# Performance work log

Hardware: AMD Instinct MI355X
Metric: run time of the kernel (lower is better)

The kernel has to match this reference:

```python
import jax, jax.numpy as jnp
import numpy as np

B, N, F, H, E = 8, 10000, 256, 128, 320000
P_DROP = 0.5

def setup_inputs() -> dict:
    key = jax.random.key(0)
    kx, ku, kr, kc, kv, kw = jax.random.split(key, 6)
    x = jax.random.normal(kx, (B, N, F), dtype=jnp.float32)
    drop_u = jax.random.uniform(ku, (B, N, F), dtype=jnp.float32)
    rows = jax.random.randint(kr, (B, E), 0, N, dtype=jnp.int64)
    cols = jax.random.randint(kc, (B, E), 0, N, dtype=jnp.int64)
    vals = jax.random.uniform(kv, (B, E), dtype=jnp.float32)
    weight = jax.random.normal(kw, (F, H), dtype=jnp.float32)
    return {"x": x, "drop_u": drop_u, "rows": rows, "cols": cols, "vals": vals, "weight": weight}

def _spmm(rows, cols, vals, dense):
    # out[r] += vals * dense[c]  -> A @ dense for one graph
    gathered = vals[:, None] * dense[cols]          # [E, H]
    return jax.ops.segment_sum(gathered, rows, num_segments=N)  # [N, H]

def reference(x, drop_u, rows, cols, vals, weight):
    # inverted dropout, p=0.5
    mask = (drop_u > P_DROP).astype(x.dtype)
    xd = x * mask * (1.0 / (1.0 - P_DROP))          # [B, N, F]
    xw = jnp.einsum('bnf,fh->bnh', xd, weight)      # [B, N, H]
    out = jax.vmap(_spmm)(rows, cols, vals, xw)     # [B, N, H]
    return out
```

## Files before the change

kernel.cpp:

```cpp
#include <hip/hip_runtime.h>
#include <hip/hip_bf16.h>

#define DEVINL __device__ __forceinline__

constexpr int Bb = 8;
constexpr int Nn = 10000;
constexpr int Ff = 256;
constexpr int Hh = 128;
constexpr int Ee = 320000;
constexpr int Mm = Bb * Nn;

constexpr int CHUNK = 64;
constexpr int NCH = (Nn + CHUNK - 1) / CHUNK;
constexpr int CAP = 2560;
constexpr int GPB = 40;
constexpr int EPG = Ee / GPB;
constexpr int TW_BLOCKS = (Ff * Hh) / 256;

typedef __attribute__((ext_vector_type(8))) short short8;
typedef __attribute__((ext_vector_type(4))) float float4v;
typedef __attribute__((ext_vector_type(4))) unsigned short ushort4v;

DEVINL float b2f(unsigned short s) {
    unsigned int u = ((unsigned int)s) << 16;
    float f;
    __builtin_memcpy(&f, &u, 4);
    return f;
}
DEVINL unsigned short f2b(float f) {
    unsigned int u;
    __builtin_memcpy(&u, &f, 4);
    unsigned int r = (u + 0x7fffu + ((u >> 16) & 1u)) >> 16;
    return (unsigned short)r;
}
DEVINL float i2f(int i) {
    float f;
    __builtin_memcpy(&f, &i, 4);
    return f;
}

__global__ __launch_bounds__(256) void bucket_kernel(const int* __restrict__ rows,
                                                     const int* __restrict__ cols,
                                                     const float* __restrict__ vals,
                                                     int* __restrict__ cur,
                                                     int2* __restrict__ bkt,
                                                     const float* __restrict__ w,
                                                     unsigned short* __restrict__ wT) {
    int t = threadIdx.x;
    if (blockIdx.x >= Bb * GPB) {
        int idx = (blockIdx.x - Bb * GPB) * 256 + t;
        if (idx < Ff * Hh) {
            int h = idx / Ff, k = idx % Ff;
            wT[idx] = f2b(w[(size_t)k * Hh + h]);
        }
        return;
    }
    __shared__ int lcnt[NCH];
    __shared__ int lbase[NCH];
    int raw = blockIdx.x;
    int b = raw & 7;
    int g = raw >> 3;
    const int base = b * Ee + g * EPG;

    for (int j = t; j < NCH; j += 256) lcnt[j] = 0;
    __syncthreads();
    for (int i = t; i < EPG; i += 256)
        atomicAdd(&lcnt[rows[base + i] >> 6], 1);
    __syncthreads();
    for (int j = t; j < NCH; j += 256)
        lbase[j] = atomicAdd(&cur[b * NCH + j], lcnt[j]);
    __syncthreads();
    for (int j = t; j < NCH; j += 256) lcnt[j] = 0;
    __syncthreads();
    for (int i = t; i < EPG; i += 256) {
        int r = rows[base + i];
        int bk = r >> 6;
        int off = atomicAdd(&lcnt[bk], 1);
        int pos = lbase[bk] + off;
        if (pos < CAP) {
            int c = cols[base + i];
            float vf = vals[base + i];
            int vb;
            __builtin_memcpy(&vb, &vf, 4);
            bkt[(size_t)(b * NCH + bk) * CAP + pos] = make_int2(c | ((r & 63) << 20), vb);
        }
    }
}

__global__ __launch_bounds__(256, 3) void gemm_kernel(const float* __restrict__ x,
                                                      const float* __restrict__ u,
                                                      const unsigned short* __restrict__ wT,
                                                      unsigned short* __restrict__ xw) {
    __shared__ unsigned short sA[64 * 136];
    __shared__ unsigned short sB[128 * 136];
    int t = threadIdx.x;
    int wave = t >> 6, lane = t & 63;
    int n = lane & 15, q = lane >> 4;
    int m0 = blockIdx.x * 64;

    float4v acc[8];
#pragma unroll
    for (int i = 0; i < 8; i++) acc[i] = {0.f, 0.f, 0.f, 0.f};

    for (int kh = 0; kh < 2; kh++) {
#pragma unroll
        for (int i = 0; i < 8; i++) {
            int idx = t + i * 256;
            int row = idx >> 5;
            int c4 = idx & 31;
            const float* xp = x + (size_t)(m0 + row) * Ff + kh * 128 + c4 * 4;
            const float* up = u + (size_t)(m0 + row) * Ff + kh * 128 + c4 * 4;
            float4 xv = *(const float4*)xp;
            float4 uv = *(const float4*)up;
            ushort4v a;
            a.x = f2b(uv.x > 0.5f ? xv.x * 2.0f : 0.0f);
            a.y = f2b(uv.y > 0.5f ? xv.y * 2.0f : 0.0f);
            a.z = f2b(uv.z > 0.5f ? xv.z * 2.0f : 0.0f);
            a.w = f2b(uv.w > 0.5f ? xv.w * 2.0f : 0.0f);
            *(ushort4v*)(&sA[row * 136 + c4 * 4]) = a;
        }
#pragma unroll
        for (int i = 0; i < 8; i++) {
            int idx = t + i * 256;
            int h = idx >> 4;
            int kc = idx & 15;
            short8 bv = *(const short8*)(wT + (size_t)h * Ff + kh * 128 + kc * 8);
            *(short8*)(&sB[h * 136 + kc * 8]) = bv;
        }
        __syncthreads();
#pragma unroll
        for (int k0 = 0; k0 < 128; k0 += 32) {
            short8 af = *(const short8*)(&sA[(wave * 16 + n) * 136 + k0 + q * 8]);
#pragma unroll
            for (int tt = 0; tt < 8; tt++) {
                short8 bf = *(const short8*)(&sB[(tt * 16 + n) * 136 + k0 + q * 8]);
                acc[tt] = __builtin_amdgcn_mfma_f32_16x16x32_bf16(af, bf, acc[tt], 0, 0, 0);
            }
        }
        __syncthreads();
    }
#pragma unroll
    for (int tt = 0; tt < 8; tt++) {
#pragma unroll
        for (int r = 0; r < 4; r++) {
            int row = m0 + wave * 16 + q * 4 + r;
            int col = tt * 16 + n;
            xw[(size_t)row * Hh + col] = f2b(acc[tt][r]);
        }
    }
}

__global__ __launch_bounds__(256) void spmm_kernel(const int* __restrict__ cur,
                                                   const int2* __restrict__ bkt,
                                                   const unsigned short* __restrict__ xw,
                                                   float* __restrict__ out) {
    __shared__ int2 sedge[CAP];
    __shared__ int scnt[CHUNK];
    __shared__ int soff[CHUNK];
    __shared__ int scur[CHUNK];
    int raw = blockIdx.x;
    int blk = (raw & 7) * NCH + (raw >> 3);
    int b = blk / NCH, ch = blk % NCH;
    int t = threadIdx.x, w = t >> 6, lane = t & 63;

    if (t < CHUNK) scnt[t] = 0;
    __syncthreads();
    int cnt = cur[blk];
    if (cnt > CAP) cnt = CAP;
    const int2* pe = bkt + (size_t)blk * CAP;

    for (int i = t; i < cnt; i += 256)
        atomicAdd(&scnt[pe[i].x >> 20], 1);
    __syncthreads();
    if (w == 0) {
        int v = scnt[lane];
        int s = v;
#pragma unroll
        for (int d = 1; d < 64; d <<= 1) {
            int o = __shfl_up(s, d);
            if (lane >= d) s += o;
        }
        soff[lane] = s - v;
        scur[lane] = s - v;
    }
    __syncthreads();
    for (int i = t; i < cnt; i += 256) {
        int2 e = pe[i];
        int pos = atomicAdd(&scur[e.x >> 20], 1);
        sedge[pos] = e;
    }
    __syncthreads();

    const unsigned short* xwb = xw + (size_t)b * Nn * Hh;
    for (int rr = 0; rr < 16; rr++) {
        int rl = w * 16 + rr;
        int r = ch * CHUNK + rl;
        if (r >= Nn) break;
        int off = soff[rl];
        int rcnt = scnt[rl];

        float a0[8], a1[8];
#pragma unroll
        for (int k = 0; k < 8; k++) { a0[k] = 0.f; a1[k] = 0.f; }

        for (int c0 = 0; c0 < rcnt; c0 += 64) {
            int rem = rcnt - c0;
            if (rem > 64) rem = 64;
            int2 e = make_int2(0, 0);
            if (lane < rem) e = sedge[off + c0 + lane];
            int rrp = (rem + 7) & ~7;
            for (int j = 0; j < rrp; j += 8) {
#pragma unroll
                for (int k = 0; k < 8; k++) {
                    int c = __builtin_amdgcn_readlane(e.x, j + k) & 0xFFFFF;
                    float v = i2f(__builtin_amdgcn_readlane(e.y, j + k));
                    unsigned int two = *(const unsigned int*)(xwb + (size_t)c * Hh + lane * 2);
                    a0[k] += v * b2f((unsigned short)(two & 0xffffu));
                    a1[k] += v * b2f((unsigned short)(two >> 16));
                }
            }
        }
        float s0 = ((a0[0] + a0[1]) + (a0[2] + a0[3])) + ((a0[4] + a0[5]) + (a0[6] + a0[7]));
        float s1 = ((a1[0] + a1[1]) + (a1[2] + a1[3])) + ((a1[4] + a1[5]) + (a1[6] + a1[7]));
        float2 res;
        res.x = s0;
        res.y = s1;
        *(float2*)(out + ((size_t)b * Nn + r) * Hh + lane * 2) = res;
    }
}

extern "C" void kernel_launch(void* const* d_in, const int* in_sizes, int n_in,
                              void* d_out, int out_size, void* d_ws, size_t ws_size,
                              hipStream_t stream) {
    const float* x    = (const float*)d_in[0];
    const float* du   = (const float*)d_in[1];
    const int*   rows = (const int*)d_in[2];
    const int*   cols = (const int*)d_in[3];
    const float* vals = (const float*)d_in[4];
    const float* w    = (const float*)d_in[5];
    float*       out  = (float*)d_out;

    char* p = (char*)d_ws;
    unsigned short* xw = (unsigned short*)p; p += (size_t)Mm * Hh * 2;
    unsigned short* wT = (unsigned short*)p; p += (size_t)Ff * Hh * 2;
    int* cur   = (int*)p; p += (size_t)Bb * NCH * 4;
    int2* bkt  = (int2*)p; p += (size_t)Bb * NCH * CAP * 8;

    hipMemsetAsync(cur, 0, (size_t)Bb * NCH * 4, stream);
    bucket_kernel<<<Bb * GPB + TW_BLOCKS, 256, 0, stream>>>(rows, cols, vals, cur, bkt, w, wT);
    gemm_kernel<<<Mm / 64, 256, 0, stream>>>(x, du, wT, xw);
    spmm_kernel<<<Bb * NCH, 256, 0, stream>>>(cur, bkt, xw, out);
}
```

Baseline: 336.0 us.

## Replace chunked bucket sort with exact per-row CSR build and one-wave-per-row SpMM

Replaces the 64-row chunk bucketing, which had a fixed capacity and an in-block re-sort, with a global per-row histogram, a per-graph prefix scan and an atomic scatter into an exact CSR array. The SpMM then assigns one wave per row, stages up to 160 edges in shared memory and falls back to global reads for longer rows. Column indices are pre-shifted into byte offsets to save address arithmetic. This removes the capacity truncation and the per-block sorting work, at the cost of two extra kernel launches, global atomics on individual rows and many small blocks.

```diff
diff --git a/kernel.cpp b/kernel.cpp
--- a/kernel.cpp
+++ b/kernel.cpp
@@ -10,12 +10,10 @@
 constexpr int Ee = 320000;
 constexpr int Mm = Bb * Nn;
 
-constexpr int CHUNK = 64;
-constexpr int NCH = (Nn + CHUNK - 1) / CHUNK;
-constexpr int CAP = 2560;
 constexpr int GPB = 40;
 constexpr int EPG = Ee / GPB;
 constexpr int TW_BLOCKS = (Ff * Hh) / 256;
+constexpr int SCAP = 160;
 
 typedef __attribute__((ext_vector_type(8))) short short8;
 typedef __attribute__((ext_vector_type(4))) float float4v;
@@ -38,14 +36,23 @@
     __builtin_memcpy(&f, &i, 4);
     return f;
 }
-
-__global__ __launch_bounds__(256) void bucket_kernel(const int* __restrict__ rows,
-                                                     const int* __restrict__ cols,
-                                                     const float* __restrict__ vals,
-                                                     int* __restrict__ cur,
-                                                     int2* __restrict__ bkt,
-                                                     const float* __restrict__ w,
-                                                     unsigned short* __restrict__ wT) {
+DEVINL float lo_bf(unsigned int two) {
+    unsigned int u = two << 16;
+    float f;
+    __builtin_memcpy(&f, &u, 4);
+    return f;
+}
+DEVINL float hi_bf(unsigned int two) {
+    unsigned int u = two & 0xffff0000u;
+    float f;
+    __builtin_memcpy(&f, &u, 4);
+    return f;
+}
+
+__global__ __launch_bounds__(256) void hist_kernel(const int* __restrict__ rows,
+                                                   int* __restrict__ cnt,
+                                                   const float* __restrict__ w,
+                                                   unsigned short* __restrict__ wT) {
     int t = threadIdx.x;
     if (blockIdx.x >= Bb * GPB) {
         int idx = (blockIdx.x - Bb * GPB) * 256 + t;
@@ -55,35 +62,83 @@
         }
         return;
     }
-    __shared__ int lcnt[NCH];
-    __shared__ int lbase[NCH];
     int raw = blockIdx.x;
     int b = raw & 7;
     int g = raw >> 3;
     const int base = b * Ee + g * EPG;
-
-    for (int j = t; j < NCH; j += 256) lcnt[j] = 0;
+    int* cb = cnt + b * Nn;
+    for (int i = t; i < EPG; i += 256)
+        atomicAdd(&cb[rows[base + i]], 1);
+}
+
+__global__ __launch_bounds__(1024) void scan_kernel(const int* __restrict__ cnt,
+                                                    int* __restrict__ off,
+                                                    int* __restrict__ cur) {
+    __shared__ int wsum[16];
+    int b = blockIdx.x;
+    int t = threadIdx.x;
+    int lane = t & 63, w = t >> 6;
+    const int base = b * Nn;
+    int local[10];
+    int s = 0;
+    int r0 = t * 10;
+#pragma unroll
+    for (int j = 0; j < 10; j++) {
+        int r = r0 + j;
+        int c = (r < Nn) ? cnt[base + r] : 0;
+        local[j] = s;
+        s += c;
+    }
+    int incl = s;
+#pragma unroll
+    for (int d = 1; d < 64; d <<= 1) {
+        int o = __shfl_up(incl, d);
+        if (lane >= d) incl += o;
+    }
+    if (lane == 63) wsum[w] = incl;
     __syncthreads();
-    for (int i = t; i < EPG; i += 256)
-        atomicAdd(&lcnt[rows[base + i] >> 6], 1);
+    if (w == 0) {
+        int v = (lane < 16) ? wsum[lane] : 0;
+        int sc = v;
+#pragma unroll
+        for (int d = 1; d < 16; d <<= 1) {
+            int o = __shfl_up(sc, d);
+            if (lane >= d) sc += o;
+        }
+        if (lane < 16) wsum[lane] = sc - v;
+    }
     __syncthreads();
-    for (int j = t; j < NCH; j += 256)
-        lbase[j] = atomicAdd(&cur[b * NCH + j], lcnt[j]);
-    __syncthreads();
-    for (int j = t; j < NCH; j += 256) lcnt[j] = 0;
-    __syncthreads();
+    int tbase = b * Ee + wsum[w] + (incl - s);
+#pragma unroll
+    for (int j = 0; j < 10; j++) {
+        int r = r0 + j;
+        if (r < Nn) {
+            int o = tbase + local[j];
+            off[base + r] = o;
+            cur[base + r] = o;
+        }
+    }
+}
+
+__global__ __launch_bounds__(256) void scatter_kernel(const int* __restrict__ rows,
+                                                      const int* __restrict__ cols,
+                                                      const float* __restrict__ vals,
+                                                      int* __restrict__ cur,
+                                                      int2* __restrict__ csr) {
+    int raw = blockIdx.x;
+    int b = raw & 7;
+    int g = raw >> 3;
+    int t = threadIdx.x;
+    const int base = b * Ee + g * EPG;
+    int* cb = cur + b * Nn;
     for (int i = t; i < EPG; i += 256) {
         int r = rows[base + i];
-        int bk = r >> 6;
-        int off = atomicAdd(&lcnt[bk], 1);
-        int pos = lbase[bk] + off;
-        if (pos < CAP) {
-            int c = cols[base + i];
-            float vf = vals[base + i];
-            int vb;
-            __builtin_memcpy(&vb, &vf, 4);
-            bkt[(size_t)(b * NCH + bk) * CAP + pos] = make_int2(c | ((r & 63) << 20), vb);
-        }
+        int c = cols[base + i];
+        float vf = vals[base + i];
+        int vb;
+        __builtin_memcpy(&vb, &vf, 4);
+        int pos = atomicAdd(&cb[r], 1);
+        csr[pos] = make_int2(c << 8, vb);
     }
 }
 
@@ -150,83 +205,56 @@
     }
 }
 
-__global__ __launch_bounds__(256) void spmm_kernel(const int* __restrict__ cur,
-                                                   const int2* __restrict__ bkt,
+__global__ __launch_bounds__(256) void spmm_kernel(const int* __restrict__ off,
+                                                   const int* __restrict__ cnt,
+                                                   const int2* __restrict__ csr,
                                                    const unsigned short* __restrict__ xw,
                                                    float* __restrict__ out) {
-    __shared__ int2 sedge[CAP];
-    __shared__ int scnt[CHUNK];
-    __shared__ int soff[CHUNK];
-    __shared__ int scur[CHUNK];
+    __shared__ int2 sE[4 * SCAP];
     int raw = blockIdx.x;
-    int blk = (raw & 7) * NCH + (raw >> 3);
-    int b = blk / NCH, ch = blk % NCH;
+    int b = raw & 7;
+    int rchunk = raw >> 3;
     int t = threadIdx.x, w = t >> 6, lane = t & 63;
-
-    if (t < CHUNK) scnt[t] = 0;
+    int row = rchunk * 4 + w;
+    int gi = b * Nn + row;
+    int o0 = off[gi];
+    int rc = cnt[gi];
+    int cstage = rc < SCAP ? rc : SCAP;
+    int2* slot = sE + w * SCAP;
+    for (int i = lane; i < cstage; i += 64) slot[i] = csr[o0 + i];
+    int c4 = (cstage + 3) & ~3;
+    for (int i = cstage + lane; i < c4; i += 64) slot[i] = make_int2(0, 0);
     __syncthreads();
-    int cnt = cur[blk];
-    if (cnt > CAP) cnt = CAP;
-    const int2* pe = bkt + (size_t)blk * CAP;
-
-    for (int i = t; i < cnt; i += 256)
-        atomicAdd(&scnt[pe[i].x >> 20], 1);
-    __syncthreads();
-    if (w == 0) {
-        int v = scnt[lane];
-        int s = v;
-#pragma unroll
-        for (int d = 1; d < 64; d <<= 1) {
-            int o = __shfl_up(s, d);
-            if (lane >= d) s += o;
-        }
-        soff[lane] = s - v;
-        scur[lane] = s - v;
-    }
-    __syncthreads();
-    for (int i = t; i < cnt; i += 256) {
-        int2 e = pe[i];
-        int pos = atomicAdd(&scur[e.x >> 20], 1);
-        sedge[pos] = e;
-    }
-    __syncthreads();
-
-    const unsigned short* xwb = xw + (size_t)b * Nn * Hh;
-    for (int rr = 0; rr < 16; rr++) {
-        int rl = w * 16 + rr;
-        int r = ch * CHUNK + rl;
-        if (r >= Nn) break;
-        int off = soff[rl];
-        int rcnt = scnt[rl];
-
-        float a0[8], a1[8];
-#pragma unroll
-        for (int k = 0; k < 8; k++) { a0[k] = 0.f; a1[k] = 0.f; }
-
-        for (int c0 = 0; c0 < rcnt; c0 += 64) {
-            int rem = rcnt - c0;
-            if (rem > 64) rem = 64;
-            int2 e = make_int2(0, 0);
-            if (lane < rem) e = sedge[off + c0 + lane];
-            int rrp = (rem + 7) & ~7;
-            for (int j = 0; j < rrp; j += 8) {
-#pragma unroll
-                for (int k = 0; k < 8; k++) {
-                    int c = __builtin_amdgcn_readlane(e.x, j + k) & 0xFFFFF;
-                    float v = i2f(__builtin_amdgcn_readlane(e.y, j + k));
-                    unsigned int two = *(const unsigned int*)(xwb + (size_t)c * Hh + lane * 2);
-                    a0[k] += v * b2f((unsigned short)(two & 0xffffu));
-                    a1[k] += v * b2f((unsigned short)(two >> 16));
-                }
-            }
-        }
-        float s0 = ((a0[0] + a0[1]) + (a0[2] + a0[3])) + ((a0[4] + a0[5]) + (a0[6] + a0[7]));
-        float s1 = ((a1[0] + a1[1]) + (a1[2] + a1[3])) + ((a1[4] + a1[5]) + (a1[6] + a1[7]));
-        float2 res;
-        res.x = s0;
-        res.y = s1;
-        *(float2*)(out + ((size_t)b * Nn + r) * Hh + lane * 2) = res;
-    }
+
+    const char* xwb = (const char*)(xw + (size_t)b * Nn * Hh);
+    int lane4 = lane * 4;
+    float a0[4], a1[4];
+#pragma unroll
+    for (int k = 0; k < 4; k++) { a0[k] = 0.f; a1[k] = 0.f; }
+
+    for (int i = 0; i < c4; i += 4) {
+#pragma unroll
+        for (int k = 0; k < 4; k++) {
+            int2 e = slot[i + k];
+            unsigned int two = *(const unsigned int*)(xwb + (unsigned)(e.x + lane4));
+            float v = i2f(e.y);
+            a0[k] += v * lo_bf(two);
+            a1[k] += v * hi_bf(two);
+        }
+    }
+    for (int i = SCAP; i < rc; i++) {
+        int2 e = csr[o0 + i];
+        unsigned int two = *(const unsigned int*)(xwb + (unsigned)(e.x + lane4));
+        float v = i2f(e.y);
+        a0[0] += v * lo_bf(two);
+        a1[0] += v * hi_bf(two);
+    }
+    float s0 = (a0[0] + a0[1]) + (a0[2] + a0[3]);
+    float s1 = (a1[0] + a1[1]) + (a1[2] + a1[3]);
+    float2 res;
+    res.x = s0;
+    res.y = s1;
+    *(float2*)(out + ((size_t)b * Nn + row) * Hh + lane * 2) = res;
 }
 
 extern "C" void kernel_launch(void* const* d_in, const int* in_sizes, int n_in,
@@ -243,11 +271,15 @@
     char* p = (char*)d_ws;
     unsigned short* xw = (unsigned short*)p; p += (size_t)Mm * Hh * 2;
     unsigned short* wT = (unsigned short*)p; p += (size_t)Ff * Hh * 2;
-    int* cur   = (int*)p; p += (size_t)Bb * NCH * 4;
-    int2* bkt  = (int2*)p; p += (size_t)Bb * NCH * CAP * 8;
-
-    hipMemsetAsync(cur, 0, (size_t)Bb * NCH * 4, stream);
-    bucket_kernel<<<Bb * GPB + TW_BLOCKS, 256, 0, stream>>>(rows, cols, vals, cur, bkt, w, wT);
+    int* cnt  = (int*)p; p += (size_t)Mm * 4;
+    int* off  = (int*)p; p += (size_t)Mm * 4;
+    int* cur  = (int*)p; p += (size_t)Mm * 4;
+    int2* csr = (int2*)p; p += (size_t)Bb * Ee * 8;
+
+    hipMemsetAsync(cnt, 0, (size_t)Mm * 4, stream);
+    hist_kernel<<<Bb * GPB + TW_BLOCKS, 256, 0, stream>>>(rows, cnt, w, wT);
+    scan_kernel<<<Bb, 1024, 0, stream>>>(cnt, off, cur);
+    scatter_kernel<<<Bb * GPB, 256, 0, stream>>>(rows, cols, vals, cur, csr);
     gemm_kernel<<<Mm / 64, 256, 0, stream>>>(x, du, wT, xw);
-    spmm_kernel<<<Bb * NCH, 256, 0, stream>>>(cur, bkt, xw, out);
-}
+    spmm_kernel<<<Bb * 2500, 256, 0, stream>>>(off, cnt, csr, xw, out);
+}
```

Result: slower. 488.6 us (+45.4%).

## Stage bucketed edges in shared memory and simplify SpMM edge loop

Applied to the files above, without the earlier changes.

The bucket kernel now sorts each block's edges locally in shared memory by chunk, using a block-wide prefix scan, before writing them out. Edges for the same bucket therefore land in contiguous global slots instead of scattered ones, and the number of edge groups per graph doubles. Edges are repacked so the column is pre-shifted into a byte offset and the local row sits in the top bits. The SpMM inner loop reads edges directly from LDS per row with four accumulators instead of broadcasting via readlane, which cuts padding work and index arithmetic but adds LDS loads per edge.

```diff
diff --git a/kernel.cpp b/kernel.cpp
--- a/kernel.cpp
+++ b/kernel.cpp
@@ -13,7 +13,7 @@
 constexpr int CHUNK = 64;
 constexpr int NCH = (Nn + CHUNK - 1) / CHUNK;
 constexpr int CAP = 2560;
-constexpr int GPB = 40;
+constexpr int GPB = 80;
 constexpr int EPG = Ee / GPB;
 constexpr int TW_BLOCKS = (Ff * Hh) / 256;
 
@@ -21,12 +21,6 @@
 typedef __attribute__((ext_vector_type(4))) float float4v;
 typedef __attribute__((ext_vector_type(4))) unsigned short ushort4v;
 
-DEVINL float b2f(unsigned short s) {
-    unsigned int u = ((unsigned int)s) << 16;
-    float f;
-    __builtin_memcpy(&f, &u, 4);
-    return f;
-}
 DEVINL unsigned short f2b(float f) {
     unsigned int u;
     __builtin_memcpy(&u, &f, 4);
@@ -38,14 +32,26 @@
     __builtin_memcpy(&f, &i, 4);
     return f;
 }
-
-__global__ __launch_bounds__(256) void bucket_kernel(const int* __restrict__ rows,
-                                                     const int* __restrict__ cols,
-                                                     const float* __restrict__ vals,
-                                                     int* __restrict__ cur,
-                                                     int2* __restrict__ bkt,
-                                                     const float* __restrict__ w,
-                                                     unsigned short* __restrict__ wT) {
+DEVINL float lo_bf(unsigned int two) {
+    unsigned int u = two << 16;
+    float f;
+    __builtin_memcpy(&f, &u, 4);
+    return f;
+}
+DEVINL float hi_bf(unsigned int two) {
+    unsigned int u = two & 0xffff0000u;
+    float f;
+    __builtin_memcpy(&f, &u, 4);
+    return f;
+}
+
+__global__ __launch_bounds__(256) void bucket2_kernel(const int* __restrict__ rows,
+                                                      const int* __restrict__ cols,
+                                                      const float* __restrict__ vals,
+                                                      int* __restrict__ cur,
+                                                      int2* __restrict__ bkt,
+                                                      const float* __restrict__ w,
+                                                      unsigned short* __restrict__ wT) {
     int t = threadIdx.x;
     if (blockIdx.x >= Bb * GPB) {
         int idx = (blockIdx.x - Bb * GPB) * 256 + t;
@@ -55,8 +61,12 @@
         }
         return;
     }
+    __shared__ int2 sedge[EPG];
     __shared__ int lcnt[NCH];
-    __shared__ int lbase[NCH];
+    __shared__ int lofs[NCH];
+    __shared__ int lcur[NCH];
+    __shared__ int gall[NCH];
+    __shared__ int wsum[4];
     int raw = blockIdx.x;
     int b = raw & 7;
     int g = raw >> 3;
@@ -67,23 +77,52 @@
     for (int i = t; i < EPG; i += 256)
         atomicAdd(&lcnt[rows[base + i] >> 6], 1);
     __syncthreads();
-    for (int j = t; j < NCH; j += 256)
-        lbase[j] = atomicAdd(&cur[b * NCH + j], lcnt[j]);
-    __syncthreads();
-    for (int j = t; j < NCH; j += 256) lcnt[j] = 0;
+    {
+        int lane = t & 63, wv = t >> 6;
+        int v = (t < NCH) ? lcnt[t] : 0;
+        int incl = v;
+#pragma unroll
+        for (int d = 1; d < 64; d <<= 1) {
+            int o = __shfl_up(incl, d);
+            if (lane >= d) incl += o;
+        }
+        if (lane == 63) wsum[wv] = incl;
+        __syncthreads();
+        if (t == 0) {
+            int s = 0;
+#pragma unroll
+            for (int k = 0; k < 4; k++) { int x = wsum[k]; wsum[k] = s; s += x; }
+        }
+        __syncthreads();
+        if (t < NCH) {
+            int ex = incl - v + wsum[wv];
+            lofs[t] = ex;
+            lcur[t] = ex;
+        }
+    }
+    __syncthreads();
+    for (int j = t; j < NCH; j += 256) {
+        int gb = atomicAdd(&cur[b * NCH + j], lcnt[j]);
+        gall[j] = gb - lofs[j];
+    }
     __syncthreads();
     for (int i = t; i < EPG; i += 256) {
         int r = rows[base + i];
+        int c = cols[base + i];
+        float vf = vals[base + i];
+        int vb;
+        __builtin_memcpy(&vb, &vf, 4);
         int bk = r >> 6;
-        int off = atomicAdd(&lcnt[bk], 1);
-        int pos = lbase[bk] + off;
-        if (pos < CAP) {
-            int c = cols[base + i];
-            float vf = vals[base + i];
-            int vb;
-            __builtin_memcpy(&vb, &vf, 4);
-            bkt[(size_t)(b * NCH + bk) * CAP + pos] = make_int2(c | ((r & 63) << 20), vb);
-        }
+        int p = atomicAdd(&lcur[bk], 1);
+        sedge[p] = make_int2(((r & 63) << 26) | (c << 8) | bk, vb);
+    }
+    __syncthreads();
+    for (int i = t; i < EPG; i += 256) {
+        int2 e = sedge[i];
+        int j = e.x & 0xff;
+        int slot = gall[j] + i;
+        if (slot < CAP)
+            bkt[(size_t)(b * NCH + j) * CAP + slot] = e;
     }
 }
 
@@ -154,74 +193,76 @@
                                                    const int2* __restrict__ bkt,
                                                    const unsigned short* __restrict__ xw,
                                                    float* __restrict__ out) {
-    __shared__ int2 sedge[CAP];
-    __shared__ int scnt[CHUNK];
-    __shared__ int soff[CHUNK];
-    __shared__ int scur[CHUNK];
+    __shared__ int2 ssort[CAP];
+    __shared__ int rh[CHUNK];
+    __shared__ int roff[CHUNK];
+    __shared__ int rcur[CHUNK];
     int raw = blockIdx.x;
     int blk = (raw & 7) * NCH + (raw >> 3);
     int b = blk / NCH, ch = blk % NCH;
     int t = threadIdx.x, w = t >> 6, lane = t & 63;
 
-    if (t < CHUNK) scnt[t] = 0;
+    if (t < CHUNK) rh[t] = 0;
     __syncthreads();
     int cnt = cur[blk];
     if (cnt > CAP) cnt = CAP;
     const int2* pe = bkt + (size_t)blk * CAP;
 
     for (int i = t; i < cnt; i += 256)
-        atomicAdd(&scnt[pe[i].x >> 20], 1);
+        atomicAdd(&rh[((unsigned)pe[i].x) >> 26], 1);
     __syncthreads();
     if (w == 0) {
-        int v = scnt[lane];
+        int v = rh[lane];
         int s = v;
 #pragma unroll
         for (int d = 1; d < 64; d <<= 1) {
             int o = __shfl_up(s, d);
             if (lane >= d) s += o;
         }
-        soff[lane] = s - v;
-        scur[lane] = s - v;
+        roff[lane] = s - v;
+        rcur[lane] = s - v;
     }
     __syncthreads();
     for (int i = t; i < cnt; i += 256) {
         int2 e = pe[i];
-        int pos = atomicAdd(&scur[e.x >> 20], 1);
-        sedge[pos] = e;
-    }
-    __syncthreads();
-
-    const unsigned short* xwb = xw + (size_t)b * Nn * Hh;
+        int p = atomicAdd(&rcur[((unsigned)e.x) >> 26], 1);
+        ssort[p] = make_int2(e.x & 0x3FFF00, e.y);
+    }
+    __syncthreads();
+
+    const char* xwb = (const char*)(xw + (size_t)b * Nn * Hh);
+    int lane4 = lane * 4;
     for (int rr = 0; rr < 16; rr++) {
         int rl = w * 16 + rr;
         int r = ch * CHUNK + rl;
         if (r >= Nn) break;
-        int off = soff[rl];
-        int rcnt = scnt[rl];
-
-        float a0[8], a1[8];
-#pragma unroll
-        for (int k = 0; k < 8; k++) { a0[k] = 0.f; a1[k] = 0.f; }
-
-        for (int c0 = 0; c0 < rcnt; c0 += 64) {
-            int rem = rcnt - c0;
-            if (rem > 64) rem = 64;
-            int2 e = make_int2(0, 0);
-            if (lane < rem) e = sedge[off + c0 + lane];
-            int rrp = (rem + 7) & ~7;
-            for (int j = 0; j < rrp; j += 8) {
-#pragma unroll
-                for (int k = 0; k < 8; k++) {
-                    int c = __builtin_amdgcn_readlane(e.x, j + k) & 0xFFFFF;
-                    float v = i2f(__builtin_amdgcn_readlane(e.y, j + k));
-                    unsigned int two = *(const unsigned int*)(xwb + (size_t)c * Hh + lane * 2);
-                    a0[k] += v * b2f((unsigned short)(two & 0xffffu));
-                    a1[k] += v * b2f((unsigned short)(two >> 16));
-                }
+        int off = roff[rl];
+        int rcnt = rh[rl];
+
+        float a0[4], a1[4];
+#pragma unroll
+        for (int k = 0; k < 4; k++) { a0[k] = 0.f; a1[k] = 0.f; }
+
+        int mn = rcnt & ~3;
+        for (int i = 0; i < mn; i += 4) {
+#pragma unroll
+            for (int k = 0; k < 4; k++) {
+                int2 e = ssort[off + i + k];
+                unsigned int two = *(const unsigned int*)(xwb + (unsigned)(e.x + lane4));
+                float v = i2f(e.y);
+                a0[k] += v * lo_bf(two);
+                a1[k] += v * hi_bf(two);
             }
         }
-        float s0 = ((a0[0] + a0[1]) + (a0[2] + a0[3])) + ((a0[4] + a0[5]) + (a0[6] + a0[7]));
-        float s1 = ((a1[0] + a1[1]) + (a1[2] + a1[3])) + ((a1[4] + a1[5]) + (a1[6] + a1[7]));
+        for (int i = mn; i < rcnt; i++) {
+            int2 e = ssort[off + i];
+            unsigned int two = *(const unsigned int*)(xwb + (unsigned)(e.x + lane4));
+            float v = i2f(e.y);
+            a0[i - mn] += v * lo_bf(two);
+            a1[i - mn] += v * hi_bf(two);
+        }
+        float s0 = (a0[0] + a0[1]) + (a0[2] + a0[3]);
+        float s1 = (a1[0] + a1[1]) + (a1[2] + a1[3]);
         float2 res;
         res.x = s0;
         res.y = s1;
@@ -247,7 +288,7 @@
     int2* bkt  = (int2*)p; p += (size_t)Bb * NCH * CAP * 8;
 
     hipMemsetAsync(cur, 0, (size_t)Bb * NCH * 4, stream);
-    bucket_kernel<<<Bb * GPB + TW_BLOCKS, 256, 0, stream>>>(rows, cols, vals, cur, bkt, w, wT);
+    bucket2_kernel<<<Bb * GPB + TW_BLOCKS, 256, 0, stream>>>(rows, cols, vals, cur, bkt, w, wT);
     gemm_kernel<<<Mm / 64, 256, 0, stream>>>(x, du, wT, xw);
     spmm_kernel<<<Bb * NCH, 256, 0, stream>>>(cur, bkt, xw, out);
 }
```

Measured after the change: 288.9 us. 1.16x faster.
